# Kernel optimization log

Measured on AMD Instinct MI355X. Metric: run time of the kernel, lower is better.

## Reference

```python
import jax, jax.numpy as jnp
import numpy as np

E, H, I = 8, 2048, 768  # num_experts, hidden_size, moe_intermediate_size
B, S = 4, 1024


def setup_inputs() -> dict:
    key = jax.random.key(0)
    k1, k2, k3, k4, k5 = jax.random.split(key, 5)
    hidden_states = jax.random.normal(k1, (B, S, H), dtype=jnp.float32)
    routing_weights = jax.random.uniform(k2, (B * S, E), dtype=jnp.float32)
    router_indices = jax.random.randint(k3, (B * S, 2), 0, E)
    gate_up_proj = jax.random.normal(k4, (E, H, 2 * I), dtype=jnp.float32) * 0.02
    down_proj = jax.random.normal(k5, (E, I, H), dtype=jnp.float32) * 0.02
    return {
        "hidden_states": hidden_states,
        "routing_weights": routing_weights,
        "router_indices": router_indices,
        "gate_up_proj": gate_up_proj,
        "down_proj": down_proj,
    }


def reference(hidden_states, routing_weights, router_indices, gate_up_proj, down_proj):
    b, s, h = hidden_states.shape
    x = hidden_states.reshape(-1, h)  # [T, H], T = B*S
    # dense all-experts: every token through every expert
    gate_up = jnp.einsum("th,ehd->etd", x, gate_up_proj)  # [E, T, 2I]
    gate, up = jnp.split(gate_up, 2, axis=-1)
    inter = up * jax.nn.silu(gate)  # [E, T, I]
    out = jnp.einsum("eti,eih->eth", inter, down_proj)  # [E, T, H]
    rw = routing_weights.T.reshape(out.shape[0], b, s)  # [E, B, S]
    out = out.reshape(out.shape[0], b, s, h) * rw[..., None]
    return out.sum(axis=0)  # [B, S, H]
```

## Files before the change

### kernel.cpp

```cpp
#include <hip/hip_runtime.h>
#include <cstdint>
#include <cstddef>

#define NE 8
#define NH 2048
#define NI 768
#define NT 4096
#define NK2 6144

typedef __bf16 bf16x8 __attribute__((ext_vector_type(8)));
typedef float f32x4 __attribute__((ext_vector_type(4)));
typedef unsigned short u16x8 __attribute__((ext_vector_type(8)));

__device__ __forceinline__ unsigned short f2bf(float f) {
  unsigned int u = __builtin_bit_cast(unsigned int, f);
  u += 0x7fffu + ((u >> 16) & 1u);
  return (unsigned short)(u >> 16);
}

__device__ __forceinline__ void gload_lds16(const void* g, void* s) {
  __builtin_amdgcn_global_load_lds(
      (const __attribute__((address_space(1))) unsigned int*)g,
      (__attribute__((address_space(3))) unsigned int*)s, 16, 0, 0);
}

__global__ __launch_bounds__(256) void k_cvt(const float* __restrict__ in,
                                             unsigned short* __restrict__ out,
                                             long n) {
  long i = ((long)blockIdx.x * blockDim.x + threadIdx.x) * 8;
  if (i >= n) return;
  float4 f0 = *reinterpret_cast<const float4*>(in + i);
  float4 f1 = *reinterpret_cast<const float4*>(in + i + 4);
  u16x8 o;
  o[0] = f2bf(f0.x); o[1] = f2bf(f0.y); o[2] = f2bf(f0.z); o[3] = f2bf(f0.w);
  o[4] = f2bf(f1.x); o[5] = f2bf(f1.y); o[6] = f2bf(f1.z); o[7] = f2bf(f1.w);
  *reinterpret_cast<u16x8*>(out + i) = o;
}

__global__ __launch_bounds__(256) void k_transpose_cvt(
    const float* __restrict__ in, unsigned short* __restrict__ out,
    int R, int C, long inBS, long outBS, int outCS, int mode) {
  __shared__ float tile[32][33];
  const int b = blockIdx.z;
  const int r0 = blockIdx.y * 32, c0 = blockIdx.x * 32;
  const int tx = threadIdx.x, ty = threadIdx.y;
  const float* ib = in + (long)b * inBS;
#pragma unroll
  for (int d = 0; d < 4; d++)
    tile[ty + d * 8][tx] = ib[(long)(r0 + ty + d * 8) * C + c0 + tx];
  __syncthreads();
#pragma unroll
  for (int d = 0; d < 4; d++) {
    int c = c0 + ty + d * 8;
    int r = r0 + tx;
    int orow;
    if (mode == 1) {
      int z = (c >= NI) ? 1 : 0;
      int cc = c - z * NI;
      orow = ((cc >> 4) << 5) + (z << 4) + (cc & 15);
    } else {
      orow = c;
    }
    out[(long)b * outBS + (long)orow * outCS + r] = f2bf(tile[tx][ty + d * 8]);
  }
}


__global__ __launch_bounds__(512, 1) void k_gemm1(
    const unsigned short* __restrict__ Xb,
    const unsigned short* __restrict__ W1t,
    const float* __restrict__ rw,
    unsigned short* __restrict__ inter) {
  __shared__ unsigned short lds[4][16384];

  const int e = blockIdx.z;
  const int t0 = blockIdx.y * 256;
  const int bn = blockIdx.x;
  const int tid = threadIdx.x;
  const int lane = tid & 63, wave = tid >> 6;
  const int wr = wave >> 2, wc = wave & 3;
  const int fr = lane & 15, fq = lane >> 4;
  const int nkt = NH / 32;

  const unsigned short* Bg = W1t + (size_t)e * (2 * NI) * NH;

  int r0c, k0c, r1c, k1c;
  {
    int c = tid, pr = c >> 3, pc = c & 7, pcl = pc ^ (pr & 7);
    r0c = (pr << 1) | (pcl >> 2); k0c = pcl & 3;
    c = tid + 512; pr = c >> 3; pc = c & 7; pcl = pc ^ (pr & 7);
    r1c = (pr << 1) | (pcl >> 2); k1c = pcl & 3;
  }
  const unsigned short* sA0 = Xb + (size_t)(t0 + r0c) * NH + k0c * 8;
  const unsigned short* sA1 = Xb + (size_t)(t0 + r1c) * NH + k1c * 8;
  const unsigned short* sB0 = Bg + (size_t)(bn * 256 + r0c) * NH + k0c * 8;
  const unsigned short* sB1 = Bg + (size_t)(bn * 256 + r1c) * NH + k1c * 8;
  const int dst0 = tid * 8, dst1 = tid * 8 + 4096;

#define STG1(T) do { \
    unsigned short* L_ = lds[(T) & 3]; const size_t ko_ = (size_t)(T) * 32; \
    gload_lds16(sA0 + ko_, L_ + dst0); \
    gload_lds16(sA1 + ko_, L_ + dst1); \
    gload_lds16(sB0 + ko_, L_ + 8192 + dst0); \
    gload_lds16(sB1 + ko_, L_ + 8192 + dst1); \
  } while (0)

  f32x4 acc[8][4];
#pragma unroll
  for (int i = 0; i < 8; ++i)
#pragma unroll
    for (int j = 0; j < 4; ++j) acc[i][j] = (f32x4){0.f, 0.f, 0.f, 0.f};

  int aoff[8], boff[4];
#pragma unroll
  for (int m = 0; m < 8; ++m) {
    const int rA = (m >> 2) * 128 + wr * 64 + (m & 3) * 16 + fr;
    const int pr = rA >> 1;
    const int pcs = (((rA & 1) << 2) | fq) ^ (pr & 7);
    aoff[m] = pr * 64 + pcs * 8;
  }
#pragma unroll
  for (int j = 0; j < 4; ++j) {
    const int rB = (j >> 1) * 128 + wc * 32 + (j & 1) * 16 + fr;
    const int pr = rB >> 1;
    const int pcs = (((rB & 1) << 2) | fq) ^ (pr & 7);
    boff[j] = 8192 + pr * 64 + pcs * 8;
  }

#define READ1(T, F) do { \
    const unsigned short* L_ = lds[(T) & 3]; \
    _Pragma("unroll") \
    for (int m = 0; m < 8; ++m) F[m] = *reinterpret_cast<const bf16x8*>(L_ + aoff[m]); \
    _Pragma("unroll") \
    for (int j = 0; j < 4; ++j) F[8 + j] = *reinterpret_cast<const bf16x8*>(L_ + boff[j]); \
  } while (0)

#define REGION1(KT, CUR, NXT) do { \
    const int kt_ = (KT); \
    if (kt_ + 1 < nkt) READ1(kt_ + 1, NXT); \
    if (kt_ + 3 < nkt) STG1(kt_ + 3); \
    _Pragma("unroll") \
    for (int m = 0; m < 8; ++m) \
      _Pragma("unroll") \
      for (int j = 0; j < 4; ++j) \
        acc[m][j] = __builtin_amdgcn_mfma_f32_16x16x32_bf16(CUR[m], CUR[8 + j], acc[m][j], 0, 0, 0); \
    if (kt_ + 3 < nkt)      { asm volatile("s_waitcnt vmcnt(4)" ::: "memory"); } \
    else if (kt_ + 2 < nkt) { asm volatile("s_waitcnt vmcnt(0)" ::: "memory"); } \
    if (kt_ + 1 < nkt)      { asm volatile("s_barrier" ::: "memory"); } \
  } while (0)

  STG1(0); STG1(1); STG1(2);
  asm volatile("s_waitcnt vmcnt(4)" ::: "memory");
  asm volatile("s_barrier" ::: "memory");

  bf16x8 fE[12], fO[12];
  READ1(0, fE);
  for (int i = 0; i < nkt / 2; ++i) {
    REGION1(2 * i, fE, fO);
    REGION1(2 * i + 1, fO, fE);
  }
  asm volatile("s_waitcnt vmcnt(0)" ::: "memory");
#undef REGION1
#undef READ1
#undef STG1

#pragma unroll
  for (int i = 0; i < 8; ++i) {
    const int trow = t0 + (i >> 2) * 128 + wr * 64 + (i & 3) * 16 + fq * 4;
#pragma unroll
    for (int r = 0; r < 4; ++r) {
      const int t = trow + r;
      const float rwv = rw[(size_t)t * NE + e];
#pragma unroll
      for (int p = 0; p < 2; ++p) {
        float g = acc[i][2 * p][r];
        float u = acc[i][2 * p + 1][r];
        float s = g / (1.f + __expf(-g));
        const int col = bn * 128 + (p * 4 + wc) * 16 + fr;
        inter[(size_t)t * NK2 + e * NI + col] = f2bf(rwv * u * s);
      }
    }
  }
}

__global__ __launch_bounds__(512, 1) void k_gemm2(
    const unsigned short* __restrict__ inter,
    const unsigned short* __restrict__ W2t,
    float* __restrict__ out) {
  __shared__ unsigned short lds[4][12288];

  const int t0 = blockIdx.y * 256;
  const int h0 = blockIdx.x * 128;
  const int tid = threadIdx.x;
  const int lane = tid & 63, wave = tid >> 6;
  const int wr = wave >> 1, wc = wave & 1;
  const int fr = lane & 15, fq = lane >> 4;
  const int nkt = NK2 / 32;

  int r0c, k0c, r1c, k1c;
  {
    int c = tid, pr = c >> 3, pc = c & 7, pcl = pc ^ (pr & 7);
    r0c = (pr << 1) | (pcl >> 2); k0c = pcl & 3;
    c = tid + 512; pr = c >> 3; pc = c & 7; pcl = pc ^ (pr & 7);
    r1c = (pr << 1) | (pcl >> 2); k1c = pcl & 3;
  }
  const unsigned short* sA0 = inter + (size_t)(t0 + r0c) * NK2 + k0c * 8;
  const unsigned short* sA1 = inter + (size_t)(t0 + r1c) * NK2 + k1c * 8;
  const unsigned short* sB0 = W2t + (size_t)(h0 + r0c) * NK2 + k0c * 8;
  const int dst0 = tid * 8, dst1 = tid * 8 + 4096;

#define STG2(T) do { \
    unsigned short* L_ = lds[(T) & 3]; const size_t ko_ = (size_t)(T) * 32; \
    gload_lds16(sA0 + ko_, L_ + dst0); \
    gload_lds16(sA1 + ko_, L_ + dst1); \
    gload_lds16(sB0 + ko_, L_ + 8192 + dst0); \
  } while (0)

  f32x4 acc[4][4];
#pragma unroll
  for (int i = 0; i < 4; ++i)
#pragma unroll
    for (int j = 0; j < 4; ++j) acc[i][j] = (f32x4){0.f, 0.f, 0.f, 0.f};

  int aoff[4], boff[4];
#pragma unroll
  for (int m = 0; m < 4; ++m) {
    const int rA = wr * 64 + m * 16 + fr;
    const int pr = rA >> 1;
    const int pcs = (((rA & 1) << 2) | fq) ^ (pr & 7);
    aoff[m] = pr * 64 + pcs * 8;
  }
#pragma unroll
  for (int j = 0; j < 4; ++j) {
    const int rB = wc * 64 + j * 16 + fr;
    const int pr = rB >> 1;
    const int pcs = (((rB & 1) << 2) | fq) ^ (pr & 7);
    boff[j] = 8192 + pr * 64 + pcs * 8;
  }

#define READ2(T, F) do { \
    const unsigned short* L_ = lds[(T) & 3]; \
    _Pragma("unroll") \
    for (int m = 0; m < 4; ++m) F[m] = *reinterpret_cast<const bf16x8*>(L_ + aoff[m]); \
    _Pragma("unroll") \
    for (int j = 0; j < 4; ++j) F[4 + j] = *reinterpret_cast<const bf16x8*>(L_ + boff[j]); \
  } while (0)

#define REGION2(KT, CUR, NXT) do { \
    const int kt_ = (KT); \
    if (kt_ + 1 < nkt) READ2(kt_ + 1, NXT); \
    if (kt_ + 3 < nkt) STG2(kt_ + 3); \
    _Pragma("unroll") \
    for (int m = 0; m < 4; ++m) \
      _Pragma("unroll") \
      for (int j = 0; j < 4; ++j) \
        acc[m][j] = __builtin_amdgcn_mfma_f32_16x16x32_bf16(CUR[m], CUR[4 + j], acc[m][j], 0, 0, 0); \
    if (kt_ + 3 < nkt)      { asm volatile("s_waitcnt vmcnt(3)" ::: "memory"); } \
    else if (kt_ + 2 < nkt) { asm volatile("s_waitcnt vmcnt(0)" ::: "memory"); } \
    if (kt_ + 1 < nkt)      { asm volatile("s_barrier" ::: "memory"); } \
  } while (0)

  STG2(0); STG2(1); STG2(2);
  asm volatile("s_waitcnt vmcnt(3)" ::: "memory");
  asm volatile("s_barrier" ::: "memory");

  bf16x8 fE[8], fO[8];
  READ2(0, fE);
  for (int i = 0; i < nkt / 2; ++i) {
    REGION2(2 * i, fE, fO);
    REGION2(2 * i + 1, fO, fE);
  }
  asm volatile("s_waitcnt vmcnt(0)" ::: "memory");
#undef REGION2
#undef READ2
#undef STG2

  const int rowBase = t0 + wr * 64 + fq * 4;
#pragma unroll
  for (int i = 0; i < 4; ++i)
#pragma unroll
    for (int j = 0; j < 4; ++j)
#pragma unroll
      for (int r = 0; r < 4; ++r)
        out[(size_t)(rowBase + i * 16 + r) * NH + h0 + wc * 64 + j * 16 + fr] =
            acc[i][j][r];
}

extern "C" void kernel_launch(void* const* d_in, const int* in_sizes, int n_in,
                              void* d_out, int out_size, void* d_ws, size_t ws_size,
                              hipStream_t stream) {
  const float* x = (const float*)d_in[0];
  const float* rw = (const float*)d_in[1];
  const float* w1 = (const float*)d_in[3];
  const float* w2 = (const float*)d_in[4];
  float* out = (float*)d_out;

  char* ws = (char*)d_ws;
  unsigned short* Xb = (unsigned short*)ws;
  unsigned short* W1t = (unsigned short*)(ws + 16777216);
  unsigned short* W2t = (unsigned short*)(ws + 16777216 + 50331648);
  unsigned short* inter = (unsigned short*)(ws + 16777216 + 50331648 + 25165824);

  k_cvt<<<dim3((NT * NH) / (256 * 8)), dim3(256), 0, stream>>>(x, Xb, (long)NT * NH);
  k_transpose_cvt<<<dim3((2 * NI) / 32, NH / 32, NE), dim3(32, 8), 0, stream>>>(
      w1, W1t, NH, 2 * NI, (long)NH * 2 * NI, (long)2 * NI * NH, NH, 1);
  k_transpose_cvt<<<dim3(NH / 32, NI / 32, NE), dim3(32, 8), 0, stream>>>(
      w2, W2t, NI, NH, (long)NI * NH, (long)NI, NK2, 0);
  k_gemm1<<<dim3((2 * NI) / 256, NT / 256, NE), dim3(512), 0, stream>>>(Xb, W1t, rw, inter);
  k_gemm2<<<dim3(NH / 128, NT / 256), dim3(512), 0, stream>>>(inter, W2t, out);
}
```

Before: 363.0 us.

## Switch both GEMMs to 32x32x16 MFMA tiles with matching gate/up interleave

Replaces the 16x16x32 bf16 MFMA instructions in both GEMM kernels with 32x32x16 MFMAs. The LDS fragment offsets, accumulator layout and epilogue indexing are rewritten to match, and the weight transpose now interleaves gate and up in 32-row groups instead of 16. The larger MFMA shape is meant to cut LDS fragment reads per FLOP and instruction-issue overhead. s_setprio around the MFMA block is added to favour math issue. The cost is different register pressure and a less coalesced store pattern in the epilogue.

```diff
diff --git a/kernel.cpp b/kernel.cpp
--- a/kernel.cpp
+++ b/kernel.cpp
@@ -9,7 +9,7 @@
 #define NK2 6144
 
 typedef __bf16 bf16x8 __attribute__((ext_vector_type(8)));
-typedef float f32x4 __attribute__((ext_vector_type(4)));
+typedef float f32x16 __attribute__((ext_vector_type(16)));
 typedef unsigned short u16x8 __attribute__((ext_vector_type(8)));
 
 __device__ __forceinline__ unsigned short f2bf(float f) {
@@ -57,7 +57,7 @@
     if (mode == 1) {
       int z = (c >= NI) ? 1 : 0;
       int cc = c - z * NI;
-      orow = ((cc >> 4) << 5) + (z << 4) + (cc & 15);
+      orow = ((cc >> 5) << 6) + (z << 5) + (cc & 31);
     } else {
       orow = c;
     }
@@ -79,7 +79,7 @@
   const int tid = threadIdx.x;
   const int lane = tid & 63, wave = tid >> 6;
   const int wr = wave >> 2, wc = wave & 3;
-  const int fr = lane & 15, fq = lane >> 4;
+  const int cl = lane & 31, hi = lane >> 5;
   const int nkt = NH / 32;
 
   const unsigned short* Bg = W1t + (size_t)e * (2 * NI) * NH;
@@ -105,45 +105,58 @@
     gload_lds16(sB1 + ko_, L_ + 8192 + dst1); \
   } while (0)
 
-  f32x4 acc[8][4];
-#pragma unroll
-  for (int i = 0; i < 8; ++i)
-#pragma unroll
-    for (int j = 0; j < 4; ++j) acc[i][j] = (f32x4){0.f, 0.f, 0.f, 0.f};
+  f32x16 acc[4][2];
+#pragma unroll
+  for (int m = 0; m < 4; ++m)
+#pragma unroll
+    for (int j = 0; j < 2; ++j)
+#pragma unroll
+      for (int r = 0; r < 16; ++r) acc[m][j][r] = 0.f;
 
   int aoff[8], boff[4];
 #pragma unroll
-  for (int m = 0; m < 8; ++m) {
-    const int rA = (m >> 2) * 128 + wr * 64 + (m & 3) * 16 + fr;
+  for (int m = 0; m < 4; ++m) {
+    const int rA = (m >> 1) * 128 + wr * 64 + (m & 1) * 32 + cl;
     const int pr = rA >> 1;
-    const int pcs = (((rA & 1) << 2) | fq) ^ (pr & 7);
-    aoff[m] = pr * 64 + pcs * 8;
-  }
-#pragma unroll
-  for (int j = 0; j < 4; ++j) {
-    const int rB = (j >> 1) * 128 + wc * 32 + (j & 1) * 16 + fr;
+#pragma unroll
+    for (int ks = 0; ks < 2; ++ks) {
+      const int pcl = ((rA & 1) << 2) + ks * 2 + hi;
+      aoff[m * 2 + ks] = pr * 64 + (pcl ^ (pr & 7)) * 8;
+    }
+  }
+#pragma unroll
+  for (int j = 0; j < 2; ++j) {
+    const int rB = wc * 64 + j * 32 + cl;
     const int pr = rB >> 1;
-    const int pcs = (((rB & 1) << 2) | fq) ^ (pr & 7);
-    boff[j] = 8192 + pr * 64 + pcs * 8;
+#pragma unroll
+    for (int ks = 0; ks < 2; ++ks) {
+      const int pcl = ((rB & 1) << 2) + ks * 2 + hi;
+      boff[j * 2 + ks] = 8192 + pr * 64 + (pcl ^ (pr & 7)) * 8;
+    }
   }
 
 #define READ1(T, F) do { \
     const unsigned short* L_ = lds[(T) & 3]; \
     _Pragma("unroll") \
-    for (int m = 0; m < 8; ++m) F[m] = *reinterpret_cast<const bf16x8*>(L_ + aoff[m]); \
-    _Pragma("unroll") \
-    for (int j = 0; j < 4; ++j) F[8 + j] = *reinterpret_cast<const bf16x8*>(L_ + boff[j]); \
+    for (int q = 0; q < 8; ++q) F[q] = *reinterpret_cast<const bf16x8*>(L_ + aoff[q]); \
+    _Pragma("unroll") \
+    for (int q = 0; q < 4; ++q) F[8 + q] = *reinterpret_cast<const bf16x8*>(L_ + boff[q]); \
   } while (0)
 
 #define REGION1(KT, CUR, NXT) do { \
     const int kt_ = (KT); \
     if (kt_ + 1 < nkt) READ1(kt_ + 1, NXT); \
     if (kt_ + 3 < nkt) STG1(kt_ + 3); \
-    _Pragma("unroll") \
-    for (int m = 0; m < 8; ++m) \
+    __builtin_amdgcn_s_setprio(1); \
+    _Pragma("unroll") \
+    for (int ks = 0; ks < 2; ++ks) \
       _Pragma("unroll") \
-      for (int j = 0; j < 4; ++j) \
-        acc[m][j] = __builtin_amdgcn_mfma_f32_16x16x32_bf16(CUR[m], CUR[8 + j], acc[m][j], 0, 0, 0); \
+      for (int m = 0; m < 4; ++m) \
+        _Pragma("unroll") \
+        for (int j = 0; j < 2; ++j) \
+          acc[m][j] = __builtin_amdgcn_mfma_f32_32x32x16_bf16( \
+              CUR[m * 2 + ks], CUR[8 + j * 2 + ks], acc[m][j], 0, 0, 0); \
+    __builtin_amdgcn_s_setprio(0); \
     if (kt_ + 3 < nkt)      { asm volatile("s_waitcnt vmcnt(4)" ::: "memory"); } \
     else if (kt_ + 2 < nkt) { asm volatile("s_waitcnt vmcnt(0)" ::: "memory"); } \
     if (kt_ + 1 < nkt)      { asm volatile("s_barrier" ::: "memory"); } \
@@ -165,20 +178,17 @@
 #undef STG1
 
 #pragma unroll
-  for (int i = 0; i < 8; ++i) {
-    const int trow = t0 + (i >> 2) * 128 + wr * 64 + (i & 3) * 16 + fq * 4;
-#pragma unroll
-    for (int r = 0; r < 4; ++r) {
-      const int t = trow + r;
+  for (int m = 0; m < 4; ++m) {
+    const int base = t0 + (m >> 1) * 128 + wr * 64 + (m & 1) * 32 + 4 * hi;
+    const int col = bn * 128 + wc * 32 + cl;
+#pragma unroll
+    for (int r = 0; r < 16; ++r) {
+      const int t = base + (r & 3) + 8 * (r >> 2);
       const float rwv = rw[(size_t)t * NE + e];
-#pragma unroll
-      for (int p = 0; p < 2; ++p) {
-        float g = acc[i][2 * p][r];
-        float u = acc[i][2 * p + 1][r];
-        float s = g / (1.f + __expf(-g));
-        const int col = bn * 128 + (p * 4 + wc) * 16 + fr;
-        inter[(size_t)t * NK2 + e * NI + col] = f2bf(rwv * u * s);
-      }
+      float g = acc[m][0][r];
+      float u = acc[m][1][r];
+      float s = g / (1.f + __expf(-g));
+      inter[(size_t)t * NK2 + e * NI + col] = f2bf(rwv * u * s);
     }
   }
 }
@@ -194,7 +204,7 @@
   const int tid = threadIdx.x;
   const int lane = tid & 63, wave = tid >> 6;
   const int wr = wave >> 1, wc = wave & 1;
-  const int fr = lane & 15, fq = lane >> 4;
+  const int cl = lane & 31, hi = lane >> 5;
   const int nkt = NK2 / 32;
 
   int r0c, k0c, r1c, k1c;
@@ -216,45 +226,58 @@
     gload_lds16(sB0 + ko_, L_ + 8192 + dst0); \
   } while (0)
 
-  f32x4 acc[4][4];
-#pragma unroll
-  for (int i = 0; i < 4; ++i)
-#pragma unroll
-    for (int j = 0; j < 4; ++j) acc[i][j] = (f32x4){0.f, 0.f, 0.f, 0.f};
+  f32x16 acc[2][2];
+#pragma unroll
+  for (int m = 0; m < 2; ++m)
+#pragma unroll
+    for (int j = 0; j < 2; ++j)
+#pragma unroll
+      for (int r = 0; r < 16; ++r) acc[m][j][r] = 0.f;
 
   int aoff[4], boff[4];
 #pragma unroll
-  for (int m = 0; m < 4; ++m) {
-    const int rA = wr * 64 + m * 16 + fr;
+  for (int m = 0; m < 2; ++m) {
+    const int rA = wr * 64 + m * 32 + cl;
     const int pr = rA >> 1;
-    const int pcs = (((rA & 1) << 2) | fq) ^ (pr & 7);
-    aoff[m] = pr * 64 + pcs * 8;
-  }
-#pragma unroll
-  for (int j = 0; j < 4; ++j) {
-    const int rB = wc * 64 + j * 16 + fr;
+#pragma unroll
+    for (int ks = 0; ks < 2; ++ks) {
+      const int pcl = ((rA & 1) << 2) + ks * 2 + hi;
+      aoff[m * 2 + ks] = pr * 64 + (pcl ^ (pr & 7)) * 8;
+    }
+  }
+#pragma unroll
+  for (int j = 0; j < 2; ++j) {
+    const int rB = wc * 64 + j * 32 + cl;
     const int pr = rB >> 1;
-    const int pcs = (((rB & 1) << 2) | fq) ^ (pr & 7);
-    boff[j] = 8192 + pr * 64 + pcs * 8;
+#pragma unroll
+    for (int ks = 0; ks < 2; ++ks) {
+      const int pcl = ((rB & 1) << 2) + ks * 2 + hi;
+      boff[j * 2 + ks] = 8192 + pr * 64 + (pcl ^ (pr & 7)) * 8;
+    }
   }
 
 #define READ2(T, F) do { \
     const unsigned short* L_ = lds[(T) & 3]; \
     _Pragma("unroll") \
-    for (int m = 0; m < 4; ++m) F[m] = *reinterpret_cast<const bf16x8*>(L_ + aoff[m]); \
-    _Pragma("unroll") \
-    for (int j = 0; j < 4; ++j) F[4 + j] = *reinterpret_cast<const bf16x8*>(L_ + boff[j]); \
+    for (int q = 0; q < 4; ++q) F[q] = *reinterpret_cast<const bf16x8*>(L_ + aoff[q]); \
+    _Pragma("unroll") \
+    for (int q = 0; q < 4; ++q) F[4 + q] = *reinterpret_cast<const bf16x8*>(L_ + boff[q]); \
   } while (0)
 
 #define REGION2(KT, CUR, NXT) do { \
     const int kt_ = (KT); \
     if (kt_ + 1 < nkt) READ2(kt_ + 1, NXT); \
     if (kt_ + 3 < nkt) STG2(kt_ + 3); \
-    _Pragma("unroll") \
-    for (int m = 0; m < 4; ++m) \
+    __builtin_amdgcn_s_setprio(1); \
+    _Pragma("unroll") \
+    for (int ks = 0; ks < 2; ++ks) \
       _Pragma("unroll") \
-      for (int j = 0; j < 4; ++j) \
-        acc[m][j] = __builtin_amdgcn_mfma_f32_16x16x32_bf16(CUR[m], CUR[4 + j], acc[m][j], 0, 0, 0); \
+      for (int m = 0; m < 2; ++m) \
+        _Pragma("unroll") \
+        for (int j = 0; j < 2; ++j) \
+          acc[m][j] = __builtin_amdgcn_mfma_f32_32x32x16_bf16( \
+              CUR[m * 2 + ks], CUR[4 + j * 2 + ks], acc[m][j], 0, 0, 0); \
+    __builtin_amdgcn_s_setprio(0); \
     if (kt_ + 3 < nkt)      { asm volatile("s_waitcnt vmcnt(3)" ::: "memory"); } \
     else if (kt_ + 2 < nkt) { asm volatile("s_waitcnt vmcnt(0)" ::: "memory"); } \
     if (kt_ + 1 < nkt)      { asm volatile("s_barrier" ::: "memory"); } \
@@ -275,15 +298,19 @@
 #undef READ2
 #undef STG2
 
-  const int rowBase = t0 + wr * 64 + fq * 4;
-#pragma unroll
-  for (int i = 0; i < 4; ++i)
-#pragma unroll
-    for (int j = 0; j < 4; ++j)
-#pragma unroll
-      for (int r = 0; r < 4; ++r)
-        out[(size_t)(rowBase + i * 16 + r) * NH + h0 + wc * 64 + j * 16 + fr] =
-            acc[i][j][r];
+#pragma unroll
+  for (int m = 0; m < 2; ++m) {
+    const int base = t0 + wr * 64 + m * 32 + 4 * hi;
+#pragma unroll
+    for (int j = 0; j < 2; ++j) {
+      const int h = h0 + wc * 64 + j * 32 + cl;
+#pragma unroll
+      for (int r = 0; r < 16; ++r) {
+        const int t = base + (r & 3) + 8 * (r >> 2);
+        out[(size_t)t * NH + h] = acc[m][j][r];
+      }
+    }
+  }
 }
 
 extern "C" void kernel_launch(void* const* d_in, const int* in_sizes, int n_in,
```

New measurement: 411.7 us. 1.13x slower.
